# Kernel optimization log

Hardware: AMD Instinct MI355X
Metric: run time of the kernel (lower is better)

The kernel has to match this reference:

```python
import jax, jax.numpy as jnp
import numpy as np

ROWS, COLS = 4096, 2048
NUM_BITS = 4
NUM_LEVELS = 2 ** NUM_BITS  # 16
FIXED_T = 100.0
EPS = 1e-06


def setup_inputs() -> dict:
    key = jax.random.key(0)
    kw, = jax.random.split(key, 1)
    weight = jax.random.normal(kw, (ROWS, COLS), dtype=jnp.float32)
    col_min = weight.min(axis=0)
    col_max = weight.max(axis=0)
    pad = 0.01 * (col_max - col_min)
    w_min = col_min - pad  # [COLS]
    w_max = col_max + pad  # [COLS]
    return {"weight": weight, "w_min": w_min, "w_max": w_max}


def reference(weight, w_min, w_max):
    # Torch clamps against the *detached scalar* of the other bound -> stop_gradient
    w_min_c = jnp.minimum(w_min, jax.lax.stop_gradient(w_max) - EPS)          # [C]
    w_max_c = jnp.maximum(w_max, jax.lax.stop_gradient(w_min_c) + EPS)        # [C]
    rng = w_max_c - w_min_c                                                   # [C]

    q_levels = jnp.linspace(0.0, 1.0, NUM_LEVELS, dtype=weight.dtype)         # [L]

    w_norm = (weight - w_min_c[None, :]) / (rng[None, :] + EPS)               # [R, C]
    dists = -jnp.abs(w_norm[:, :, None] - q_levels[None, None, :])            # [R, C, L]
    soft_probs = jax.nn.softmax(dists * FIXED_T, axis=-1)                     # [R, C, L]

    w_q = jnp.einsum("rcl,l->rc", soft_probs, q_levels)                       # [R, C]
    w_dequant = w_q * rng[None, :] + w_min_c[None, :]                         # [R, C]

    bin_mass = soft_probs.sum(axis=0)                                         # [C, L]
    bin_probs = bin_mass / (bin_mass.sum(axis=-1, keepdims=True) + EPS)       # [C, L]
    entropy_per_col = -(bin_probs * jnp.log(bin_probs + EPS)).sum(axis=-1)    # [C]
    total_entropy = entropy_per_col.sum()

    return (w_dequant, total_entropy)
```

## Files before the change

kernel.cpp:

```cpp
#include <hip/hip_runtime.h>

#define ROWS 4096
#define COLS 2048
#define NLEV 16
#define TEMP 100.0f
#define EPS  1e-6f
#define LOG2E 1.4426950408889634f

#define TPB 256
#define RPB 32
#define RBLKS (ROWS / RPB)
#define UNROLL 8

#define RGEO 1.2726356e-3f


__global__ __launch_bounds__(TPB) void quant_main_kernel(
    const float* __restrict__ weight,
    const float* __restrict__ w_min,
    const float* __restrict__ w_max,
    float* __restrict__ dequant,
    float* __restrict__ partial)
{
    __shared__ float bins[18 * TPB];

    const int t  = threadIdx.x;
    const int c  = blockIdx.x * TPB + t;
    const int r0 = blockIdx.y * RPB;

#pragma unroll
    for (int l = 0; l < 18; ++l) bins[l * TPB + t] = 0.0f;

    const float wmin = w_min[c];
    const float wmax = w_max[c];
    const float mn   = fminf(wmin, wmax - EPS);
    const float mx   = fmaxf(wmax, mn + EPS);
    const float rng  = mx - mn;
    const float inv_rng = __builtin_amdgcn_rcpf(rng + EPS);

    const float S     = (TEMP / 15.0f) * LOG2E;
    const float invS  = 15.0f / (TEMP * LOG2E);
    const float scale = inv_rng * (TEMP * LOG2E);
    const float rng15 = rng * (1.0f / 15.0f);

    const float* __restrict__ wp = weight  + (size_t)r0 * COLS + c;
    float* __restrict__       dq = dequant + (size_t)r0 * COLS + c;

    for (int r = 0; r < RPB; r += UNROLL) {
        float w[UNROLL];
#pragma unroll
        for (int j = 0; j < UNROLL; ++j)
            w[j] = wp[(size_t)(r + j) * COLS];

#pragma unroll
        for (int j = 0; j < UNROLL; ++j) {
            const float z  = (w[j] - mn) * scale;
            float kf = floorf(z * invS);
            kf = fminf(fmaxf(kf, 0.0f), 14.0f);
            const int ki = (int)kf;
            const float f = z - kf * S;

            const float t_ = __builtin_amdgcn_exp2f(-fabsf(f));
            const float u_ = __builtin_amdgcn_exp2f(-fabsf(f - S));
            const float tl = t_ * ((kf >= 1.0f)  ? RGEO : 0.0f);
            const float uh = u_ * ((kf <= 13.0f) ? RGEO : 0.0f);

            const float s     = t_ + u_ + tl + uh;
            const float inv_s = __builtin_amdgcn_rcpf(s);
            const float ws = kf * s + (u_ - tl + 2.0f * uh);

            dq[(size_t)(r + j) * COLS] = ws * inv_s * rng15 + mn;

            const int base = ki * TPB + t;
            bins[base          ] += tl * inv_s;
            bins[base + 1 * TPB] += t_ * inv_s;
            bins[base + 2 * TPB] += u_ * inv_s;
            bins[base + 3 * TPB] += uh * inv_s;
        }
    }

    float4* pp = (float4*)(partial + ((size_t)blockIdx.y * COLS + c) * NLEV);
#pragma unroll
    for (int q = 0; q < NLEV / 4; ++q) {
        pp[q] = make_float4(bins[(q * 4 + 1) * TPB + t],
                            bins[(q * 4 + 2) * TPB + t],
                            bins[(q * 4 + 3) * TPB + t],
                            bins[(q * 4 + 4) * TPB + t]);
    }
}

__global__ __launch_bounds__(256) void reduce_kernel(
    const float* __restrict__ partial,
    float* __restrict__ reduced)
{
    const int i = blockIdx.x * 256 + threadIdx.x;
    float s = 0.0f;
#pragma unroll 4
    for (int rb = 0; rb < RBLKS; ++rb)
        s += partial[(size_t)rb * (COLS * NLEV) + i];
    reduced[i] = s;
}

__global__ __launch_bounds__(256) void entropy_kernel(
    const float* __restrict__ reduced,
    float* __restrict__ out_ent)
{
    __shared__ float red[256];
    const int t    = blockIdx.x * 256 + threadIdx.x;
    const int col  = t >> 2;
    const int quad = t & 3;

    const float4 m = *(const float4*)(reduced + (size_t)col * NLEV + quad * 4);

    float tot = m.x + m.y + m.z + m.w;
    tot += __shfl_xor(tot, 1);
    tot += __shfl_xor(tot, 2);
    const float inv = __builtin_amdgcn_rcpf(tot + EPS);

    float ent = 0.0f;
    {
        const float p0 = m.x * inv, p1 = m.y * inv, p2 = m.z * inv, p3 = m.w * inv;
        ent -= p0 * __logf(p0 + EPS);
        ent -= p1 * __logf(p1 + EPS);
        ent -= p2 * __logf(p2 + EPS);
        ent -= p3 * __logf(p3 + EPS);
    }

    red[threadIdx.x] = ent;
    __syncthreads();
#pragma unroll
    for (int off = 128; off > 0; off >>= 1) {
        if (threadIdx.x < off) red[threadIdx.x] += red[threadIdx.x + off];
        __syncthreads();
    }
    if (threadIdx.x == 0) atomicAdd(out_ent, red[0]);
}

extern "C" void kernel_launch(void* const* d_in, const int* in_sizes, int n_in,
                              void* d_out, int out_size, void* d_ws, size_t ws_size,
                              hipStream_t stream)
{
    const float* weight = (const float*)d_in[0];
    const float* w_min  = (const float*)d_in[1];
    const float* w_max  = (const float*)d_in[2];

    float* out     = (float*)d_out;
    float* dequant = out;
    float* out_ent = out + (size_t)ROWS * COLS;
    float* partial = (float*)d_ws;
    float* reduced = partial + (size_t)RBLKS * COLS * NLEV;

    hipMemsetAsync(out_ent, 0, sizeof(float), stream);

    quant_main_kernel<<<dim3(COLS / TPB, RBLKS), TPB, 0, stream>>>(
        weight, w_min, w_max, dequant, partial);

    reduce_kernel<<<(COLS * NLEV) / 256, 256, 0, stream>>>(partial, reduced);

    entropy_kernel<<<(COLS * 4) / 256, 256, 0, stream>>>(reduced, out_ent);
}
```

Before: 108.4 us.

## Fuse reduce and entropy kernels, store fp16 partials, cut LDS bin updates

Merges the reduce and entropy kernels into one, which removes a launch and the intermediate reduced buffer. The per-block partial histograms are stored as fp16 to halve their traffic. The inner loop now does two LDS accumulations instead of four by keeping separate t and u bin arrays and applying the geometric neighbour weights once at the end. Other changes: the memset is replaced by a zero-store inside the main kernel, the block size drops to 128, and a few expressions become FMAs. Risks: fp16 partials lose precision for the entropy, and zeroing out_ent inside the main kernel relies on ordering against the later atomicAdd kernel.

Result: faster. 100.2 us (-7.5%).

```diff
diff --git a/kernel.cpp b/kernel.cpp
--- a/kernel.cpp
+++ b/kernel.cpp
@@ -6,13 +6,15 @@
 #define TEMP 100.0f
 #define EPS  1e-6f
 #define LOG2E 1.4426950408889634f
+#define RGEO 1.2726356e-3f
 
-#define TPB 256
+#define TPB 128
 #define RPB 32
 #define RBLKS (ROWS / RPB)
 #define UNROLL 8
 
-#define RGEO 1.2726356e-3f
+typedef _Float16 half8_t __attribute__((ext_vector_type(8)));
+typedef _Float16 half2_t __attribute__((ext_vector_type(2)));
 
 
 __global__ __launch_bounds__(TPB) void quant_main_kernel(
@@ -20,16 +22,19 @@
     const float* __restrict__ w_min,
     const float* __restrict__ w_max,
     float* __restrict__ dequant,
-    float* __restrict__ partial)
+    _Float16* __restrict__ partial,
+    float* __restrict__ out_ent)
 {
-    __shared__ float bins[18 * TPB];
+    __shared__ float bins[34 * TPB];
 
     const int t  = threadIdx.x;
     const int c  = blockIdx.x * TPB + t;
     const int r0 = blockIdx.y * RPB;
 
+    if (blockIdx.x == 0 && blockIdx.y == 0 && t == 0) out_ent[0] = 0.0f;
+
 #pragma unroll
-    for (int l = 0; l < 18; ++l) bins[l * TPB + t] = 0.0f;
+    for (int l = 0; l < 34; ++l) bins[l * TPB + t] = 0.0f;
 
     const float wmin = w_min[c];
     const float wmax = w_max[c];
@@ -41,6 +46,7 @@
     const float S     = (TEMP / 15.0f) * LOG2E;
     const float invS  = 15.0f / (TEMP * LOG2E);
     const float scale = inv_rng * (TEMP * LOG2E);
+    const float zb    = -mn * scale;
     const float rng15 = rng * (1.0f / 15.0f);
 
     const float* __restrict__ wp = weight  + (size_t)r0 * COLS + c;
@@ -54,77 +60,72 @@
 
 #pragma unroll
         for (int j = 0; j < UNROLL; ++j) {
-            const float z  = (w[j] - mn) * scale;
+            const float z  = fmaf(w[j], scale, zb);
             float kf = floorf(z * invS);
             kf = fminf(fmaxf(kf, 0.0f), 14.0f);
             const int ki = (int)kf;
-            const float f = z - kf * S;
+            const float f = fmaf(-kf, S, z);
 
             const float t_ = __builtin_amdgcn_exp2f(-fabsf(f));
             const float u_ = __builtin_amdgcn_exp2f(-fabsf(f - S));
-            const float tl = t_ * ((kf >= 1.0f)  ? RGEO : 0.0f);
-            const float uh = u_ * ((kf <= 13.0f) ? RGEO : 0.0f);
+            const float e1 = (kf >= 1.0f)  ? RGEO : 0.0f;
+            const float e2 = (kf <= 13.0f) ? RGEO : 0.0f;
+            const float t1 = t_ * e1;
+            const float u2 = u_ * e2;
+            const float s  = (t_ + t1) + (u_ + u2);
+            const float inv_s = __builtin_amdgcn_rcpf(s);
+            const float ws = fmaf(kf, s, u_) + fmaf(2.0f, u2, -t1);
 
-            const float s     = t_ + u_ + tl + uh;
-            const float inv_s = __builtin_amdgcn_rcpf(s);
-            const float ws = kf * s + (u_ - tl + 2.0f * uh);
-
-            dq[(size_t)(r + j) * COLS] = ws * inv_s * rng15 + mn;
+            dq[(size_t)(r + j) * COLS] = fmaf(ws * inv_s, rng15, mn);
 
             const int base = ki * TPB + t;
-            bins[base          ] += tl * inv_s;
-            bins[base + 1 * TPB] += t_ * inv_s;
-            bins[base + 2 * TPB] += u_ * inv_s;
-            bins[base + 3 * TPB] += uh * inv_s;
+            bins[base           ] += t_ * inv_s;
+            bins[base + 19 * TPB] += u_ * inv_s;
         }
     }
 
-    float4* pp = (float4*)(partial + ((size_t)blockIdx.y * COLS + c) * NLEV);
+    float a[17], b[17];
 #pragma unroll
-    for (int q = 0; q < NLEV / 4; ++q) {
-        pp[q] = make_float4(bins[(q * 4 + 1) * TPB + t],
-                            bins[(q * 4 + 2) * TPB + t],
-                            bins[(q * 4 + 3) * TPB + t],
-                            bins[(q * 4 + 4) * TPB + t]);
+    for (int l = 0; l < 17; ++l) a[l] = bins[l * TPB + t];
+#pragma unroll
+    for (int l = 0; l < 17; ++l) b[l] = bins[(17 + l) * TPB + t];
+
+    half8_t v0, v1;
+#pragma unroll
+    for (int l = 0; l < 16; ++l) {
+        const float bin = (a[l] + b[l + 1]) + RGEO * (a[l + 1] + b[l]);
+        if (l < 8) v0[l] = (_Float16)bin; else v1[l - 8] = (_Float16)bin;
     }
+    half8_t* pp = (half8_t*)(partial + ((size_t)blockIdx.y * COLS + c) * NLEV);
+    pp[0] = v0;
+    pp[1] = v1;
 }
 
-__global__ __launch_bounds__(256) void reduce_kernel(
-    const float* __restrict__ partial,
-    float* __restrict__ reduced)
-{
-    const int i = blockIdx.x * 256 + threadIdx.x;
-    float s = 0.0f;
-#pragma unroll 4
-    for (int rb = 0; rb < RBLKS; ++rb)
-        s += partial[(size_t)rb * (COLS * NLEV) + i];
-    reduced[i] = s;
-}
-
-__global__ __launch_bounds__(256) void entropy_kernel(
-    const float* __restrict__ reduced,
+__global__ __launch_bounds__(256) void reduce_entropy_kernel(
+    const _Float16* __restrict__ partial,
     float* __restrict__ out_ent)
 {
     __shared__ float red[256];
-    const int t    = blockIdx.x * 256 + threadIdx.x;
-    const int col  = t >> 2;
-    const int quad = t & 3;
+    const int i = blockIdx.x * 256 + threadIdx.x;
+    const half2_t* p2 = (const half2_t*)partial;
 
-    const float4 m = *(const float4*)(reduced + (size_t)col * NLEV + quad * 4);
+    float m0 = 0.0f, m1 = 0.0f;
+#pragma unroll 4
+    for (int rb = 0; rb < RBLKS; ++rb) {
+        const half2_t v = p2[(size_t)rb * (COLS * NLEV / 2) + i];
+        m0 += (float)v[0];
+        m1 += (float)v[1];
+    }
 
-    float tot = m.x + m.y + m.z + m.w;
+    float tot = m0 + m1;
     tot += __shfl_xor(tot, 1);
     tot += __shfl_xor(tot, 2);
+    tot += __shfl_xor(tot, 4);
     const float inv = __builtin_amdgcn_rcpf(tot + EPS);
 
-    float ent = 0.0f;
-    {
-        const float p0 = m.x * inv, p1 = m.y * inv, p2 = m.z * inv, p3 = m.w * inv;
-        ent -= p0 * __logf(p0 + EPS);
-        ent -= p1 * __logf(p1 + EPS);
-        ent -= p2 * __logf(p2 + EPS);
-        ent -= p3 * __logf(p3 + EPS);
-    }
+    const float p0 = m0 * inv;
+    const float p1 = m1 * inv;
+    float ent = -(p0 * __logf(p0 + EPS) + p1 * __logf(p1 + EPS));
 
     red[threadIdx.x] = ent;
     __syncthreads();
@@ -147,15 +148,11 @@
     float* out     = (float*)d_out;
     float* dequant = out;
     float* out_ent = out + (size_t)ROWS * COLS;
-    float* partial = (float*)d_ws;
-    float* reduced = partial + (size_t)RBLKS * COLS * NLEV;
-
-    hipMemsetAsync(out_ent, 0, sizeof(float), stream);
+    _Float16* partial = (_Float16*)d_ws;
 
     quant_main_kernel<<<dim3(COLS / TPB, RBLKS), TPB, 0, stream>>>(
-        weight, w_min, w_max, dequant, partial);
+        weight, w_min, w_max, dequant, partial, out_ent);
 
-    reduce_kernel<<<(COLS * NLEV) / 256, 256, 0, stream>>>(partial, reduced);
-
-    entropy_kernel<<<(COLS * 4) / 256, 256, 0, stream>>>(reduced, out_ent);
+    reduce_entropy_kernel<<<(COLS * NLEV / 2) / 256, 256, 0, stream>>>(
+        partial, out_ent);
 }
```
